# Performance work log

Hardware: AMD Instinct MI355X
Metric: run time of the kernel (lower is better)

Reference implementation:

```python
import jax, jax.numpy as jnp
import numpy as np

N = 100000   # nodes
E = 1600000  # edges (before self-loops)
D_IN = 128
HID = 64
H1 = 4       # heads of conv1
OUT = 2
EPS = 1e-5
NEG_SLOPE = 0.2


def setup_inputs():
    key = jax.random.key(0)
    ks = jax.random.split(key, 12)
    s = 0.1
    return {
        "x": jax.random.normal(ks[0], (N, D_IN), jnp.float32),
        "edge_index": jax.random.randint(ks[1], (2, E), 0, N, jnp.int64),
        "W1": jax.random.normal(ks[2], (D_IN, H1 * HID), jnp.float32) * s,
        "att_src1": jax.random.normal(ks[3], (H1, HID), jnp.float32) * s,
        "att_dst1": jax.random.normal(ks[4], (H1, HID), jnp.float32) * s,
        "b1": jnp.zeros((H1 * HID,), jnp.float32),
        "g1": jnp.ones((H1 * HID,), jnp.float32),
        "be1": jnp.zeros((H1 * HID,), jnp.float32),
        "W2": jax.random.normal(ks[5], (H1 * HID, HID), jnp.float32) * s,
        "att_src2": jax.random.normal(ks[6], (1, HID), jnp.float32) * s,
        "att_dst2": jax.random.normal(ks[7], (1, HID), jnp.float32) * s,
        "b2": jnp.zeros((HID,), jnp.float32),
        "g2": jnp.ones((HID,), jnp.float32),
        "be2": jnp.zeros((HID,), jnp.float32),
        "Wc1": jax.random.normal(ks[8], (HID, HID // 2), jnp.float32) * s,
        "bc1": jnp.zeros((HID // 2,), jnp.float32),
        "Wc2": jax.random.normal(ks[9], (HID // 2, OUT), jnp.float32) * s,
        "bc2": jnp.zeros((OUT,), jnp.float32),
    }


def _gat(x, W, a_src, a_dst, bias, src, dst, heads):
    n = x.shape[0]
    h = (x @ W).reshape(n, heads, -1)              # [N,H,C]
    e_src = jnp.einsum('nhc,hc->nh', h, a_src)     # [N,H]
    e_dst = jnp.einsum('nhc,hc->nh', h, a_dst)
    e = jax.nn.leaky_relu(e_src[src] + e_dst[dst], NEG_SLOPE)  # [Etot,H]
    m = jax.ops.segment_max(e, dst, num_segments=n)            # edge-softmax over incoming
    p = jnp.exp(e - m[dst])
    z = jax.ops.segment_sum(p, dst, num_segments=n)
    alpha = p / z[dst]
    msg = alpha[:, :, None] * h[src]               # [Etot,H,C]
    out = jax.ops.segment_sum(msg, dst, num_segments=n)        # [N,H,C]
    return out.reshape(n, -1) + bias               # concat heads + bias


def _bn(x, g, b):
    m = x.mean(0)
    v = x.var(0)
    return g * (x - m) * jax.lax.rsqrt(v + EPS) + b


def reference(x, edge_index, W1, att_src1, att_dst1, b1, g1, be1,
              W2, att_src2, att_dst2, b2, g2, be2, Wc1, bc1, Wc2, bc2):
    n = x.shape[0]
    loops = jnp.arange(n, dtype=edge_index.dtype)
    src = jnp.concatenate([edge_index[0], loops])  # PyG add_self_loops=True
    dst = jnp.concatenate([edge_index[1], loops])

    h = _gat(x, W1, att_src1, att_dst1, b1, src, dst, H1)
    h = jax.nn.elu(_bn(h, g1, be1))                # dropout = identity (eval)
    h = _gat(h, W2, att_src2, att_dst2, b2, src, dst, 1)
    h = jax.nn.elu(_bn(h, g2, be2))
    h = jax.nn.elu(h @ Wc1 + bc1)
    logits = h @ Wc2 + bc2
    return jax.nn.log_softmax(logits, axis=1)
```

## Files before the change

kernel.cpp:

```cpp
#include <hip/hip_runtime.h>
#include <hip/hip_bf16.h>

constexpr int N_  = 100000;
constexpr int E_  = 1600000;
constexpr int PAD = 48;
constexpr int NBKT = 196;
constexpr int BCAP = 16384;

constexpr size_t P_PARAMS = 8192;
constexpr size_t OFF_WPK1 = 219904;
constexpr size_t OFF_WPK2 = 285440;
constexpr size_t OFF_DEG  = 318464;
constexpr size_t OFF_ES1  = 718464;
constexpr size_t OFF_ED1  = 2318464;
constexpr size_t OFF_ES2  = 3918464;
constexpr size_t OFF_ED2  = 4318464;
constexpr size_t OFF_CSR  = 4718464;
constexpr size_t OFF_H1   = 23918464;
constexpr size_t OFF_H2   = OFF_H1;
constexpr size_t OFF_AGG2 = OFF_H1 + 12800000;
constexpr size_t OFF_AGG1 = 75118464;
constexpr size_t OFF_BCUR = 126318464;
constexpr size_t OFF_BKT  = 126319488;

typedef unsigned short ushortT;
typedef short bf16x8 __attribute__((ext_vector_type(8)));
typedef float f32x4 __attribute__((ext_vector_type(4)));

#define DEV __device__ __forceinline__

DEV float leakyf(float x) { return x > 0.f ? x : 0.2f * x; }
DEV float eluf(float x)   { return x > 0.f ? x : __expf(x) - 1.f; }
DEV float rbf(unsigned short u) { unsigned int b = ((unsigned int)u) << 16; return __uint_as_float(b); }
DEV unsigned short f2b(float f) { __hip_bfloat16 h = __float2bfloat16(f); return *reinterpret_cast<unsigned short*>(&h); }
DEV float sel_head(float4 a, int hd) {
    float r = a.x;
    r = (hd == 1) ? a.y : r;
    r = (hd == 2) ? a.z : r;
    r = (hd == 3) ? a.w : r;
    return r;
}
DEV unsigned short sel_h4(ushort4 u, int hd) {
    unsigned short r = u.x;
    r = (hd == 1) ? u.y : r;
    r = (hd == 2) ? u.z : r;
    r = (hd == 3) ? u.w : r;
    return r;
}
DEV int eread(const int* __restrict__ ei, int mode, int idx) {
    return mode ? ei[(size_t)idx * 2] : ei[idx];
}

__global__ void k_detect2(const int* __restrict__ ei, const unsigned int* __restrict__ g1raw,
                          int* __restrict__ mode, int* __restrict__ fmode) {
    __shared__ int any;
    if (threadIdx.x == 0) any = 0;
    __syncthreads();
    if (ei[2 * threadIdx.x + 1] != 0) atomicOr(&any, 1);
    __syncthreads();
    if (threadIdx.x == 0) {
        *mode = any ? 0 : 1;
        *fmode = (g1raw[0] == 0x3F800000u) ? 0 : 1;
    }
}

struct CvtArgs { const void* src[16]; int off[17]; };
__global__ __launch_bounds__(256) void k_cvtall(CvtArgs a, float* __restrict__ dst,
                                                const int* __restrict__ fmode, int total) {
    int i = blockIdx.x * 256 + threadIdx.x;
    if (i >= total) return;
    int seg = 0;
    #pragma unroll
    for (int s2 = 1; s2 < 16; ++s2) seg += (i >= a.off[s2]);
    int j = i - a.off[seg];
    float v;
    if (*fmode) v = rbf(((const unsigned short*)a.src[seg])[j]);
    else        v = ((const float*)a.src[seg])[j];
    dst[i] = v;
}

__global__ __launch_bounds__(256) void k_packw(const float* __restrict__ pp,
                                               ushortT* __restrict__ w1, ushortT* __restrict__ w2) {
    int i = blockIdx.x * 256 + threadIdx.x;
    if (i < 32768) {
        int j = i & 7, lane = (i >> 3) & 63, ks = (i >> 9) & 3, ct = i >> 11;
        int src = (ks * 32 + ((lane >> 4) << 3) + j) * 256 + ct * 16 + (lane & 15);
        w1[i] = f2b(pp[src]);
    } else if (i < 49152) {
        int i2 = i - 32768;
        int j = i2 & 7, lane = (i2 >> 3) & 63, ks = (i2 >> 9) & 7, ct = i2 >> 12;
        int src = (ks * 32 + ((lane >> 4) << 3) + j) * 64 + ct * 16 + (lane & 15);
        w2[i2] = f2b(pp[34048 + src]);
    }
}

__global__ __launch_bounds__(256) void k_bin(const int* __restrict__ ei, const int* __restrict__ mode,
                                             unsigned int* __restrict__ bucketArr,
                                             int* __restrict__ bucketCursor) {
    __shared__ unsigned int pk[8192];
    __shared__ int cnt[256], scn[256], bse[256], cur[256], gb[256];
    int tid = threadIdx.x;
    cnt[tid] = 0;
    __syncthreads();
    int e0 = blockIdx.x * 8192;
    int m = *mode;
    #pragma unroll 4
    for (int j = 0; j < 32; ++j) {
        int e = e0 + j * 256 + tid;
        if (e < E_) atomicAdd(&cnt[eread(ei, m, E_ + e) >> 9], 1);
    }
    __syncthreads();
    int v = cnt[tid];
    scn[tid] = v;
    __syncthreads();
    for (int d = 1; d < 256; d <<= 1) {
        int t2 = (tid >= d) ? scn[tid - d] : 0;
        __syncthreads();
        scn[tid] += t2;
        __syncthreads();
    }
    int excl = scn[tid] - v;
    bse[tid] = excl;
    cur[tid] = excl;
    __syncthreads();
    #pragma unroll 4
    for (int j = 0; j < 32; ++j) {
        int e = e0 + j * 256 + tid;
        if (e < E_) {
            int s = eread(ei, m, e);
            int d = eread(ei, m, E_ + e);
            int b = d >> 9;
            int p = atomicAdd(&cur[b], 1);
            pk[p] = ((unsigned int)(d & 511) << 17) | (unsigned int)s;
        }
    }
    __syncthreads();
    if (tid < NBKT) {
        int c = cnt[tid];
        gb[tid] = (c > 0) ? atomicAdd(&bucketCursor[tid], c) : 0;
    }
    __syncthreads();
    for (int b = 0; b < NBKT; ++b) {
        int c = cnt[b];
        int lo = bse[b], g = gb[b];
        for (int i = tid; i < c; i += 256) {
            int gi = g + i;
            if (gi < BCAP) bucketArr[(size_t)b * BCAP + gi] = pk[lo + i];
        }
    }
}

__global__ __launch_bounds__(256) void k_csr(const unsigned int* __restrict__ bucketArr,
                                             const int* __restrict__ bucketCursor,
                                             int* __restrict__ csr, int* __restrict__ deg) {
    __shared__ int dl[512];
    int tid = threadIdx.x;
    int b = blockIdx.x;
    int nbase = b * 512;
    int nb = min(N_ - nbase, 512);
    if (nb <= 0) return;
    dl[tid] = 0; dl[tid + 256] = 0;
    __syncthreads();
    int c = min(bucketCursor[b], BCAP);
    const unsigned int* run = bucketArr + (size_t)b * BCAP;
    for (int i = tid; i < c; i += 256) {
        unsigned int p = run[i];
        int s = (int)(p & 0x1FFFFu);
        int dloc = (int)(p >> 17);
        int slot = atomicAdd(&dl[dloc], 1);
        if (slot < PAD - 1) csr[(size_t)(nbase + dloc) * PAD + slot] = s;
    }
    __syncthreads();
    for (int t = tid; t < nb; t += 256) {
        int n = nbase + t;
        int cd = min(dl[t], PAD - 1);
        csr[(size_t)n * PAD + cd] = n;
        deg[n] = cd + 1;
    }
}

__global__ __launch_bounds__(256) void k_gemm1f(const void* __restrict__ x, const int* __restrict__ fmode,
                                                const ushortT* __restrict__ wpk,
                                                const float* __restrict__ as1, const float* __restrict__ ad1,
                                                ushortT* __restrict__ h1,
                                                float* __restrict__ es1, float* __restrict__ ed1) {
    int tid = threadIdx.x, w = tid >> 6, lane = tid & 63;
    int l15 = lane & 15, l4 = lane >> 4;
    int row0 = blockIdx.x * 32;
    int fm = *fmode;
    bf16x8 A[2][4];
    #pragma unroll
    for (int rt = 0; rt < 2; ++rt)
        #pragma unroll
        for (int ks = 0; ks < 4; ++ks) {
            size_t off = (size_t)(row0 + rt * 16 + l15) * 128 + ks * 32 + l4 * 8;
            if (fm) {
                A[rt][ks] = *(const bf16x8*)((const ushortT*)x + off);
            } else {
                const float* xf = (const float*)x + off;
                float4 v0 = *(const float4*)xf;
                float4 v1 = *(const float4*)(xf + 4);
                A[rt][ks] = (bf16x8){(short)f2b(v0.x), (short)f2b(v0.y), (short)f2b(v0.z), (short)f2b(v0.w),
                                     (short)f2b(v1.x), (short)f2b(v1.y), (short)f2b(v1.z), (short)f2b(v1.w)};
            }
        }
    f32x4 acc[2][4];
    #pragma unroll
    for (int rt = 0; rt < 2; ++rt)
        #pragma unroll
        for (int ct = 0; ct < 4; ++ct) acc[rt][ct] = (f32x4){0.f, 0.f, 0.f, 0.f};
    const bf16x8* wp = (const bf16x8*)wpk;
    #pragma unroll
    for (int ct = 0; ct < 4; ++ct) {
        int ctg = w * 4 + ct;
        bf16x8 B0 = wp[(ctg * 4 + 0) * 64 + lane];
        bf16x8 B1 = wp[(ctg * 4 + 1) * 64 + lane];
        bf16x8 B2 = wp[(ctg * 4 + 2) * 64 + lane];
        bf16x8 B3 = wp[(ctg * 4 + 3) * 64 + lane];
        #pragma unroll
        for (int rt = 0; rt < 2; ++rt) {
            acc[rt][ct] = __builtin_amdgcn_mfma_f32_16x16x32_bf16(A[rt][0], B0, acc[rt][ct], 0, 0, 0);
            acc[rt][ct] = __builtin_amdgcn_mfma_f32_16x16x32_bf16(A[rt][1], B1, acc[rt][ct], 0, 0, 0);
            acc[rt][ct] = __builtin_amdgcn_mfma_f32_16x16x32_bf16(A[rt][2], B2, acc[rt][ct], 0, 0, 0);
            acc[rt][ct] = __builtin_amdgcn_mfma_f32_16x16x32_bf16(A[rt][3], B3, acc[rt][ct], 0, 0, 0);
        }
    }
    float asc[4], adc[4];
    #pragma unroll
    for (int ct = 0; ct < 4; ++ct) {
        asc[ct] = as1[w * 64 + ct * 16 + l15];
        adc[ct] = ad1[w * 64 + ct * 16 + l15];
    }
    float pes[2][4], ped[2][4];
    #pragma unroll
    for (int rt = 0; rt < 2; ++rt)
        #pragma unroll
        for (int r = 0; r < 4; ++r) { pes[rt][r] = 0.f; ped[rt][r] = 0.f; }
    #pragma unroll
    for (int rt = 0; rt < 2; ++rt)
        #pragma unroll
        for (int ct = 0; ct < 4; ++ct)
            #pragma unroll
            for (int r = 0; r < 4; ++r) {
                float v = acc[rt][ct][r];
                int row = row0 + rt * 16 + l4 * 4 + r;
                h1[(size_t)row * 256 + w * 64 + ct * 16 + l15] = f2b(v);
                pes[rt][r] = fmaf(v, asc[ct], pes[rt][r]);
                ped[rt][r] = fmaf(v, adc[ct], ped[rt][r]);
            }
    #pragma unroll
    for (int d = 1; d < 16; d <<= 1)
        #pragma unroll
        for (int rt = 0; rt < 2; ++rt)
            #pragma unroll
            for (int r = 0; r < 4; ++r) {
                pes[rt][r] += __shfl_xor(pes[rt][r], d);
                ped[rt][r] += __shfl_xor(ped[rt][r], d);
            }
    if (l15 == 0) {
        #pragma unroll
        for (int rt = 0; rt < 2; ++rt)
            #pragma unroll
            for (int r = 0; r < 4; ++r) {
                int row = row0 + rt * 16 + l4 * 4 + r;
                es1[row * 4 + w] = pes[rt][r];
                ed1[row * 4 + w] = ped[rt][r];
            }
    }
}

__global__ __launch_bounds__(256) void k_lagg1(const ushortT* __restrict__ h1,
                                               const float* __restrict__ es1, const float* __restrict__ ed1,
                                               const int* __restrict__ deg, const int* __restrict__ csr,
                                               const float* __restrict__ b1, ushortT* __restrict__ out) {
    __shared__ int ssrc[4][PAD];
    __shared__ ushort4 sp[4][PAD];
    int wid = threadIdx.x >> 6;
    int lane = threadIdx.x & 63;
    int n = blockIdx.x * 4 + wid;
    int cnt = deg[n];
    int start = n * PAD;
    float4 ed = ((const float4*)ed1)[n];
    float z0 = 0.f, z1 = 0.f, z2 = 0.f, z3 = 0.f;
    if (lane < cnt) {
        int s = csr[start + lane];
        ssrc[wid][lane] = s;
        float4 es = ((const float4*)es1)[s];
        float p0 = __expf(leakyf(es.x + ed.x));
        float p1 = __expf(leakyf(es.y + ed.y));
        float p2 = __expf(leakyf(es.z + ed.z));
        float p3 = __expf(leakyf(es.w + ed.w));
        sp[wid][lane] = make_ushort4(f2b(p0), f2b(p1), f2b(p2), f2b(p3));
        z0 = p0; z1 = p1; z2 = p2; z3 = p3;
    }
    #pragma unroll
    for (int d = 1; d < 64; d <<= 1) {
        z0 += __shfl_xor(z0, d); z1 += __shfl_xor(z1, d);
        z2 += __shfl_xor(z2, d); z3 += __shfl_xor(z3, d);
    }
    int half = lane >> 5, lh = lane & 31, hd = lh >> 3;
    float izh = sel_head(make_float4(1.f / z0, 1.f / z1, 1.f / z2, 1.f / z3), hd);
    float a0 = 0.f, a1 = 0.f, a2 = 0.f, a3 = 0.f, a4 = 0.f, a5 = 0.f, a6 = 0.f, a7 = 0.f;
    float c0 = 0.f, c1 = 0.f, c2 = 0.f, c3 = 0.f, c4 = 0.f, c5 = 0.f, c6 = 0.f, c7 = 0.f;
    int iters = (cnt + 1) >> 1;
    for (int t = 0; t < iters; t += 4) {
        int i0 = 2 * t + half;
        int i1 = i0 + 2, i2 = i0 + 4, i3 = i0 + 6;
        bool v0 = i0 < cnt, v1 = i1 < cnt, v2 = i2 < cnt, v3 = i3 < cnt;
        int s0 = ssrc[wid][v0 ? i0 : 0];
        int s1 = ssrc[wid][v1 ? i1 : 0];
        int s2 = ssrc[wid][v2 ? i2 : 0];
        int s3 = ssrc[wid][v3 ? i3 : 0];
        ushort4 u0 = sp[wid][v0 ? i0 : 0];
        ushort4 u1 = sp[wid][v1 ? i1 : 0];
        ushort4 u2 = sp[wid][v2 ? i2 : 0];
        ushort4 u3 = sp[wid][v3 ? i3 : 0];
        float w0 = v0 ? rbf(sel_h4(u0, hd)) * izh : 0.f;
        float w1 = v1 ? rbf(sel_h4(u1, hd)) * izh : 0.f;
        float w2 = v2 ? rbf(sel_h4(u2, hd)) * izh : 0.f;
        float w3 = v3 ? rbf(sel_h4(u3, hd)) * izh : 0.f;
        uint4 r0 = *(const uint4*)(h1 + (size_t)s0 * 256 + lh * 8);
        uint4 r1 = *(const uint4*)(h1 + (size_t)s1 * 256 + lh * 8);
        uint4 r2 = *(const uint4*)(h1 + (size_t)s2 * 256 + lh * 8);
        uint4 r3 = *(const uint4*)(h1 + (size_t)s3 * 256 + lh * 8);
        a0 = fmaf(w0, rbf((unsigned short)(r0.x & 0xffff)), a0);
        a1 = fmaf(w0, rbf((unsigned short)(r0.x >> 16)), a1);
        a2 = fmaf(w0, rbf((unsigned short)(r0.y & 0xffff)), a2);
        a3 = fmaf(w0, rbf((unsigned short)(r0.y >> 16)), a3);
        a4 = fmaf(w0, rbf((unsigned short)(r0.z & 0xffff)), a4);
        a5 = fmaf(w0, rbf((unsigned short)(r0.z >> 16)), a5);
        a6 = fmaf(w0, rbf((unsigned short)(r0.w & 0xffff)), a6);
        a7 = fmaf(w0, rbf((unsigned short)(r0.w >> 16)), a7);
        c0 = fmaf(w1, rbf((unsigned short)(r1.x & 0xffff)), c0);
        c1 = fmaf(w1, rbf((unsigned short)(r1.x >> 16)), c1);
        c2 = fmaf(w1, rbf((unsigned short)(r1.y & 0xffff)), c2);
        c3 = fmaf(w1, rbf((unsigned short)(r1.y >> 16)), c3);
        c4 = fmaf(w1, rbf((unsigned short)(r1.z & 0xffff)), c4);
        c5 = fmaf(w1, rbf((unsigned short)(r1.z >> 16)), c5);
        c6 = fmaf(w1, rbf((unsigned short)(r1.w & 0xffff)), c6);
        c7 = fmaf(w1, rbf((unsigned short)(r1.w >> 16)), c7);
        a0 = fmaf(w2, rbf((unsigned short)(r2.x & 0xffff)), a0);
        a1 = fmaf(w2, rbf((unsigned short)(r2.x >> 16)), a1);
        a2 = fmaf(w2, rbf((unsigned short)(r2.y & 0xffff)), a2);
        a3 = fmaf(w2, rbf((unsigned short)(r2.y >> 16)), a3);
        a4 = fmaf(w2, rbf((unsigned short)(r2.z & 0xffff)), a4);
        a5 = fmaf(w2, rbf((unsigned short)(r2.z >> 16)), a5);
        a6 = fmaf(w2, rbf((unsigned short)(r2.w & 0xffff)), a6);
        a7 = fmaf(w2, rbf((unsigned short)(r2.w >> 16)), a7);
        c0 = fmaf(w3, rbf((unsigned short)(r3.x & 0xffff)), c0);
        c1 = fmaf(w3, rbf((unsigned short)(r3.x >> 16)), c1);
        c2 = fmaf(w3, rbf((unsigned short)(r3.y & 0xffff)), c2);
        c3 = fmaf(w3, rbf((unsigned short)(r3.y >> 16)), c3);
        c4 = fmaf(w3, rbf((unsigned short)(r3.z & 0xffff)), c4);
        c5 = fmaf(w3, rbf((unsigned short)(r3.z >> 16)), c5);
        c6 = fmaf(w3, rbf((unsigned short)(r3.w & 0xffff)), c6);
        c7 = fmaf(w3, rbf((unsigned short)(r3.w >> 16)), c7);
    }
    a0 += c0; a1 += c1; a2 += c2; a3 += c3; a4 += c4; a5 += c5; a6 += c6; a7 += c7;
    a0 += __shfl_xor(a0, 32); a1 += __shfl_xor(a1, 32);
    a2 += __shfl_xor(a2, 32); a3 += __shfl_xor(a3, 32);
    a4 += __shfl_xor(a4, 32); a5 += __shfl_xor(a5, 32);
    a6 += __shfl_xor(a6, 32); a7 += __shfl_xor(a7, 32);
    if (half == 0) {
        float4 b0 = *(const float4*)(b1 + lh * 8);
        float4 b1v = *(const float4*)(b1 + lh * 8 + 4);
        ushort4 o0 = make_ushort4(f2b(a0 + b0.x), f2b(a1 + b0.y), f2b(a2 + b0.z), f2b(a3 + b0.w));
        ushort4 o1 = make_ushort4(f2b(a4 + b1v.x), f2b(a5 + b1v.y), f2b(a6 + b1v.z), f2b(a7 + b1v.w));
        *(ushort4*)(out + (size_t)n * 256 + lh * 8)     = o0;
        *(ushort4*)(out + (size_t)n * 256 + lh * 8 + 4) = o1;
    }
}

__global__ __launch_bounds__(256) void k_bnstats1(const ushortT* __restrict__ a, double* __restrict__ sums,
                                                  double* __restrict__ sumsq) {
    int c = threadIdx.x;
    int r0 = blockIdx.x * 256;
    int r1 = min(r0 + 256, N_);
    double s = 0.0, q = 0.0;
    for (int r = r0; r < r1; ++r) { float v = rbf(a[(size_t)r * 256 + c]); s += v; q += (double)v * v; }
    atomicAdd(&sums[c], s);
    atomicAdd(&sumsq[c], q);
}

__global__ void k_bnfin(const double* __restrict__ sums, const double* __restrict__ sumsq,
                        const float* __restrict__ g, const float* __restrict__ be,
                        float* __restrict__ s, float* __restrict__ t, int C) {
    int c = threadIdx.x;
    if (c < C) {
        double mean = sums[c] / (double)N_;
        double var = fmax(sumsq[c] / (double)N_ - mean * mean, 0.0);
        double sc = (double)g[c] / sqrt(var + 1e-5);
        s[c] = (float)sc;
        t[c] = (float)((double)be[c] - mean * sc);
    }
}

__global__ __launch_bounds__(256) void k_gemm2f(const ushortT* __restrict__ agg1,
                                                const ushortT* __restrict__ wpk2,
                                                const float* __restrict__ sc1, const float* __restrict__ tc1,
                                                const float* __restrict__ as2, const float* __restrict__ ad2,
                                                ushortT* __restrict__ h2,
                                                float* __restrict__ es2, float* __restrict__ ed2) {
    int tid = threadIdx.x, w = tid >> 6, lane = tid & 63;
    int l15 = lane & 15, l4 = lane >> 4;
    int row0 = blockIdx.x * 64;
    int arow = row0 + w * 16 + l15;
    int ar = min(arow, N_ - 1);
    bf16x8 A[8];
    #pragma unroll
    for (int ks = 0; ks < 8; ++ks) {
        const ushortT* ap = agg1 + (size_t)ar * 256 + ks * 32 + l4 * 8;
        int pi = ks * 32 + l4 * 8;
        uint4 u = *(const uint4*)ap;
        float4 s0 = *(const float4*)(sc1 + pi);
        float4 s1 = *(const float4*)(sc1 + pi + 4);
        float4 t0 = *(const float4*)(tc1 + pi);
        float4 t1 = *(const float4*)(tc1 + pi + 4);
        float e0 = eluf(fmaf(rbf((unsigned short)(u.x & 0xffff)), s0.x, t0.x));
        float e1 = eluf(fmaf(rbf((unsigned short)(u.x >> 16)),    s0.y, t0.y));
        float e2 = eluf(fmaf(rbf((unsigned short)(u.y & 0xffff)), s0.z, t0.z));
        float e3 = eluf(fmaf(rbf((unsigned short)(u.y >> 16)),    s0.w, t0.w));
        float e4 = eluf(fmaf(rbf((unsigned short)(u.z & 0xffff)), s1.x, t1.x));
        float e5 = eluf(fmaf(rbf((unsigned short)(u.z >> 16)),    s1.y, t1.y));
        float e6 = eluf(fmaf(rbf((unsigned short)(u.w & 0xffff)), s1.z, t1.z));
        float e7 = eluf(fmaf(rbf((unsigned short)(u.w >> 16)),    s1.w, t1.w));
        A[ks] = (bf16x8){(short)f2b(e0), (short)f2b(e1), (short)f2b(e2), (short)f2b(e3),
                         (short)f2b(e4), (short)f2b(e5), (short)f2b(e6), (short)f2b(e7)};
    }
    f32x4 acc[4];
    #pragma unroll
    for (int ct = 0; ct < 4; ++ct) acc[ct] = (f32x4){0.f, 0.f, 0.f, 0.f};
    const bf16x8* wp = (const bf16x8*)wpk2;
    #pragma unroll
    for (int ct = 0; ct < 4; ++ct) {
        #pragma unroll
        for (int ks = 0; ks < 8; ++ks) {
            bf16x8 B = wp[(ct * 8 + ks) * 64 + lane];
            acc[ct] = __builtin_amdgcn_mfma_f32_16x16x32_bf16(A[ks], B, acc[ct], 0, 0, 0);
        }
    }
    float asc[4], adc[4];
    #pragma unroll
    for (int ct = 0; ct < 4; ++ct) {
        asc[ct] = as2[ct * 16 + l15];
        adc[ct] = ad2[ct * 16 + l15];
    }
    float pes[4] = {0.f, 0.f, 0.f, 0.f}, ped[4] = {0.f, 0.f, 0.f, 0.f};
    #pragma unroll
    for (int ct = 0; ct < 4; ++ct)
        #pragma unroll
        for (int r = 0; r < 4; ++r) {
            float v = acc[ct][r];
            int row = row0 + w * 16 + l4 * 4 + r;
            if (row < N_) h2[(size_t)row * 64 + ct * 16 + l15] = f2b(v);
            pes[r] = fmaf(v, asc[ct], pes[r]);
            ped[r] = fmaf(v, adc[ct], ped[r]);
        }
    #pragma unroll
    for (int d = 1; d < 16; d <<= 1)
        #pragma unroll
        for (int r = 0; r < 4; ++r) {
            pes[r] += __shfl_xor(pes[r], d);
            ped[r] += __shfl_xor(ped[r], d);
        }
    if (l15 == 0) {
        #pragma unroll
        for (int r = 0; r < 4; ++r) {
            int row = row0 + w * 16 + l4 * 4 + r;
            if (row < N_) { es2[row] = pes[r]; ed2[row] = ped[r]; }
        }
    }
}

__global__ __launch_bounds__(256) void k_lagg2(const ushortT* __restrict__ h2,
                                               const float* __restrict__ es2, const float* __restrict__ ed2,
                                               const int* __restrict__ deg, const int* __restrict__ csr,
                                               const float* __restrict__ b2, float* __restrict__ out) {
    __shared__ int ssrc[4][PAD];
    __shared__ float sp[4][PAD];
    int wid = threadIdx.x >> 6;
    int lane = threadIdx.x & 63;
    int n = blockIdx.x * 4 + wid;
    int cnt = deg[n];
    int start = n * PAD;
    float ed = ed2[n];
    float z = 0.f;
    if (lane < cnt) {
        int s = csr[start + lane];
        ssrc[wid][lane] = s;
        float p = __expf(leakyf(es2[s] + ed));
        sp[wid][lane] = p;
        z = p;
    }
    #pragma unroll
    for (int d = 1; d < 64; d <<= 1) z += __shfl_xor(z, d);
    float iz = 1.f / z;
    int half = lane >> 5, lh = lane & 31;
    float a0 = 0.f, a1 = 0.f, c0 = 0.f, c1 = 0.f;
    int iters = (cnt + 1) >> 1;
    for (int t = 0; t < iters; t += 4) {
        int i0 = 2 * t + half;
        int i1 = i0 + 2, i2 = i0 + 4, i3 = i0 + 6;
        bool v0 = i0 < cnt, v1 = i1 < cnt, v2 = i2 < cnt, v3 = i3 < cnt;
        int s0 = ssrc[wid][v0 ? i0 : 0];
        int s1 = ssrc[wid][v1 ? i1 : 0];
        int s2 = ssrc[wid][v2 ? i2 : 0];
        int s3 = ssrc[wid][v3 ? i3 : 0];
        float w0 = v0 ? sp[wid][i0] * iz : 0.f;
        float w1 = v1 ? sp[wid][i1] * iz : 0.f;
        float w2 = v2 ? sp[wid][i2] * iz : 0.f;
        float w3 = v3 ? sp[wid][i3] * iz : 0.f;
        unsigned int u0 = *(const unsigned int*)(h2 + (size_t)s0 * 64 + lh * 2);
        unsigned int u1 = *(const unsigned int*)(h2 + (size_t)s1 * 64 + lh * 2);
        unsigned int u2 = *(const unsigned int*)(h2 + (size_t)s2 * 64 + lh * 2);
        unsigned int u3 = *(const unsigned int*)(h2 + (size_t)s3 * 64 + lh * 2);
        a0 = fmaf(w0, rbf((unsigned short)(u0 & 0xffff)), a0);
        a1 = fmaf(w0, rbf((unsigned short)(u0 >> 16)), a1);
        c0 = fmaf(w1, rbf((unsigned short)(u1 & 0xffff)), c0);
        c1 = fmaf(w1, rbf((unsigned short)(u1 >> 16)), c1);
        a0 = fmaf(w2, rbf((unsigned short)(u2 & 0xffff)), a0);
        a1 = fmaf(w2, rbf((unsigned short)(u2 >> 16)), a1);
        c0 = fmaf(w3, rbf((unsigned short)(u3 & 0xffff)), c0);
        c1 = fmaf(w3, rbf((unsigned short)(u3 >> 16)), c1);
    }
    a0 += c0; a1 += c1;
    a0 += __shfl_xor(a0, 32);
    a1 += __shfl_xor(a1, 32);
    if (half == 0) {
        out[(size_t)n * 64 + lh * 2 + 0] = a0 + b2[lh * 2 + 0];
        out[(size_t)n * 64 + lh * 2 + 1] = a1 + b2[lh * 2 + 1];
    }
}

__global__ __launch_bounds__(256) void k_bnstats2(const float* __restrict__ a, double* __restrict__ sums,
                                                  double* __restrict__ sumsq) {
    __shared__ double sm[256], sq[256];
    int tid = threadIdx.x;
    int c = tid & 63, rr = tid >> 6;
    int r0 = blockIdx.x * 1024;
    int r1 = min(r0 + 1024, N_);
    double s = 0.0, q = 0.0;
    for (int r = r0 + rr; r < r1; r += 4) { float v = a[(size_t)r * 64 + c]; s += v; q += (double)v * v; }
    sm[tid] = s; sq[tid] = q; __syncthreads();
    if (tid < 64) {
        s = sm[tid] + sm[tid + 64] + sm[tid + 128] + sm[tid + 192];
        q = sq[tid] + sq[tid + 64] + sq[tid + 128] + sq[tid + 192];
        atomicAdd(&sums[tid], s);
        atomicAdd(&sumsq[tid], q);
    }
}

__global__ __launch_bounds__(256) void k_cls(const float* __restrict__ agg2, const float* __restrict__ Wc1,
                                             const float* __restrict__ bc1, const float* __restrict__ Wc2,
                                             const float* __restrict__ bc2, const float* __restrict__ s2,
                                             const float* __restrict__ t2, float* __restrict__ out) {
    __shared__ float w1s[2048];
    __shared__ float w2s[64];
    __shared__ float b1s[32];
    __shared__ float b2s[2];
    __shared__ float ss[64], ts[64];
    int tid = threadIdx.x;
    for (int i = tid; i < 2048; i += 256) w1s[i] = Wc1[i];
    if (tid < 64) { w2s[tid] = Wc2[tid]; ss[tid] = s2[tid]; ts[tid] = t2[tid]; }
    if (tid < 32) b1s[tid] = bc1[tid];
    if (tid < 2)  b2s[tid] = bc2[tid];
    __syncthreads();
    int n = blockIdx.x * 256 + tid;
    if (n >= N_) return;
    float hv[64];
    const float4* rp = (const float4*)(agg2 + (size_t)n * 64);
    #pragma unroll
    for (int q = 0; q < 16; ++q) {
        float4 v = rp[q];
        float tmp[4] = {v.x, v.y, v.z, v.w};
        #pragma unroll
        for (int c4 = 0; c4 < 4; ++c4) {
            int c = q * 4 + c4;
            hv[c] = eluf(fmaf(tmp[c4], ss[c], ts[c]));
        }
    }
    float l0 = b2s[0], l1 = b2s[1];
    for (int j = 0; j < 32; ++j) {
        float a = b1s[j];
        #pragma unroll
        for (int k = 0; k < 64; ++k) a = fmaf(hv[k], w1s[k * 32 + j], a);
        float u = eluf(a);
        l0 = fmaf(u, w2s[j * 2 + 0], l0);
        l1 = fmaf(u, w2s[j * 2 + 1], l1);
    }
    float mx = fmaxf(l0, l1);
    float lse = mx + __logf(__expf(l0 - mx) + __expf(l1 - mx));
    out[(size_t)n * 2 + 0] = l0 - lse;
    out[(size_t)n * 2 + 1] = l1 - lse;
}

extern "C" void kernel_launch(void* const* d_in, const int* in_sizes, int n_in,
                              void* d_out, int out_size, void* d_ws, size_t ws_size,
                              hipStream_t stream) {
    float* out = (float*)d_out;

    char* ws = (char*)d_ws;
    double* sums1  = (double*)(ws + 0);
    double* sumsq1 = (double*)(ws + 2048);
    double* sums2  = (double*)(ws + 4096);
    double* sumsq2 = (double*)(ws + 4608);
    float* s1 = (float*)(ws + 5120), *t1 = (float*)(ws + 6144);
    float* s2 = (float*)(ws + 7168), *t2 = (float*)(ws + 7424);
    int* mode  = (int*)(ws + 7936);
    int* fmode = (int*)(ws + 7940);

    float* pp   = (float*)(ws + P_PARAMS);
    float* as1f = pp + 32768;
    float* ad1f = pp + 33024;
    float* b1f  = pp + 33280;
    float* g1f  = pp + 33536;
    float* be1f = pp + 33792;
    float* as2f = pp + 50432;
    float* ad2f = pp + 50496;
    float* b2f  = pp + 50560;
    float* g2f  = pp + 50624;
    float* be2f = pp + 50688;
    float* Wc1f = pp + 50752;
    float* bc1f = pp + 52800;
    float* Wc2f = pp + 52832;
    float* bc2f = pp + 52896;
    const int CV_TOTAL = 52898;

    ushortT* wpk1 = (ushortT*)(ws + OFF_WPK1);
    ushortT* wpk2 = (ushortT*)(ws + OFF_WPK2);
    int* deg    = (int*)(ws + OFF_DEG);
    int* csr    = (int*)(ws + OFF_CSR);
    float* es1  = (float*)(ws + OFF_ES1);
    float* ed1  = (float*)(ws + OFF_ED1);
    float* es2  = (float*)(ws + OFF_ES2);
    float* ed2  = (float*)(ws + OFF_ED2);
    ushortT* h1 = (ushortT*)(ws + OFF_H1);
    ushortT* h2 = (ushortT*)(ws + OFF_H2);
    float* agg2 = (float*)(ws + OFF_AGG2);
    ushortT* agg1 = (ushortT*)(ws + OFF_AGG1);
    int* bcur = (int*)(ws + OFF_BCUR);
    unsigned int* bkt = (unsigned int*)(ws + OFF_BKT);

    hipMemsetAsync(ws, 0, 5120, stream);
    hipMemsetAsync(bcur, 0, 1024, stream);
    k_detect2<<<1, 256, 0, stream>>>((const int*)d_in[1], (const unsigned int*)d_in[6], mode, fmode);

    CvtArgs ca;
    const int srcIdx[16] = {2,3,4,5,6,7,8,9,10,11,12,13,14,15,16,17};
    const int offsEl[17] = {0,32768,33024,33280,33536,33792,34048,50432,50496,50560,
                            50624,50688,50752,52800,52832,52896,52898};
    for (int i = 0; i < 16; ++i) ca.src[i] = d_in[srcIdx[i]];
    for (int i = 0; i < 17; ++i) ca.off[i] = offsEl[i];
    k_cvtall<<<(CV_TOTAL + 255) / 256, 256, 0, stream>>>(ca, pp, fmode, CV_TOTAL);
    k_packw <<<192, 256, 0, stream>>>(pp, wpk1, wpk2);

    k_bin<<<(E_ + 8191) / 8192, 256, 0, stream>>>((const int*)d_in[1], mode, bkt, bcur);
    k_csr<<<NBKT, 256, 0, stream>>>(bkt, bcur, csr, deg);

    k_gemm1f<<<N_ / 32, 256, 0, stream>>>(d_in[0], fmode, wpk1, as1f, ad1f, h1, es1, ed1);
    k_lagg1<<<N_ / 4, 256, 0, stream>>>(h1, es1, ed1, deg, csr, b1f, agg1);
    k_bnstats1<<<(N_ + 255) / 256, 256, 0, stream>>>(agg1, sums1, sumsq1);
    k_bnfin<<<1, 256, 0, stream>>>(sums1, sumsq1, g1f, be1f, s1, t1, 256);

    k_gemm2f<<<(N_ + 63) / 64, 256, 0, stream>>>(agg1, wpk2, s1, t1, as2f, ad2f, h2, es2, ed2);
    k_lagg2<<<N_ / 4, 256, 0, stream>>>(h2, es2, ed2, deg, csr, b2f, agg2);
    k_bnstats2<<<98, 256, 0, stream>>>(agg2, sums2, sumsq2);
    k_bnfin<<<1, 64, 0, stream>>>(sums2, sumsq2, g2f, be2f, s2, t2, 64);

    k_cls<<<(N_ + 255) / 256, 256, 0, stream>>>(agg2, Wc1f, bc1f, Wc2f, bc2f, s2, t2, out);
}
```

Baseline: 517.3 us.

## Stage GEMM1 input tile in LDS, per-wave bucket flush, merge memsets

GEMM1 now loads its 32x128 input tile into shared memory with coalesced row-contiguous loads (and bf16 conversion) before building the MFMA operands, instead of each lane gathering strided rows directly from global memory. The binning kernel's flush loop assigns buckets to waves rather than looping all 256 threads over every bucket, which cuts idle lanes and per-bucket barrier-free overhead. The bucket cursor moves into the low workspace region so that one memset replaces two. These changes add an LDS round-trip and a barrier in GEMM1.

```diff
diff --git a/kernel.cpp b/kernel.cpp
--- a/kernel.cpp
+++ b/kernel.cpp
@@ -7,21 +7,20 @@
 constexpr int NBKT = 196;
 constexpr int BCAP = 16384;
 
-constexpr size_t P_PARAMS = 8192;
-constexpr size_t OFF_WPK1 = 219904;
-constexpr size_t OFF_WPK2 = 285440;
-constexpr size_t OFF_DEG  = 318464;
-constexpr size_t OFF_ES1  = 718464;
-constexpr size_t OFF_ED1  = 2318464;
-constexpr size_t OFF_ES2  = 3918464;
-constexpr size_t OFF_ED2  = 4318464;
-constexpr size_t OFF_CSR  = 4718464;
-constexpr size_t OFF_H1   = 23918464;
+constexpr size_t P_PARAMS = 12288;
+constexpr size_t OFF_WPK1 = 224000;
+constexpr size_t OFF_WPK2 = 289536;
+constexpr size_t OFF_DEG  = 322304;
+constexpr size_t OFF_ES1  = 722304;
+constexpr size_t OFF_ED1  = 2322304;
+constexpr size_t OFF_ES2  = 3922304;
+constexpr size_t OFF_ED2  = 4322304;
+constexpr size_t OFF_CSR  = 4722304;
+constexpr size_t OFF_H1   = 23922304;
 constexpr size_t OFF_H2   = OFF_H1;
 constexpr size_t OFF_AGG2 = OFF_H1 + 12800000;
-constexpr size_t OFF_AGG1 = 75118464;
-constexpr size_t OFF_BCUR = 126318464;
-constexpr size_t OFF_BKT  = 126319488;
+constexpr size_t OFF_AGG1 = 75122304;
+constexpr size_t OFF_BKT  = 126322304;
 
 typedef unsigned short ushortT;
 typedef short bf16x8 __attribute__((ext_vector_type(8)));
@@ -140,10 +139,11 @@
         gb[tid] = (c > 0) ? atomicAdd(&bucketCursor[tid], c) : 0;
     }
     __syncthreads();
-    for (int b = 0; b < NBKT; ++b) {
+    int wv = tid >> 6, ln = tid & 63;
+    for (int b = wv; b < NBKT; b += 4) {
         int c = cnt[b];
         int lo = bse[b], g = gb[b];
-        for (int i = tid; i < c; i += 256) {
+        for (int i = ln; i < c; i += 64) {
             int gi = g + i;
             if (gi < BCAP) bucketArr[(size_t)b * BCAP + gi] = pk[lo + i];
         }
@@ -184,26 +184,36 @@
                                                 const float* __restrict__ as1, const float* __restrict__ ad1,
                                                 ushortT* __restrict__ h1,
                                                 float* __restrict__ es1, float* __restrict__ ed1) {
+    __shared__ ushortT xs[32][132];
     int tid = threadIdx.x, w = tid >> 6, lane = tid & 63;
     int l15 = lane & 15, l4 = lane >> 4;
     int row0 = blockIdx.x * 32;
-    int fm = *fmode;
+    if (*fmode) {
+        const ushortT* xg = (const ushortT*)x + (size_t)row0 * 128;
+        for (int i = tid; i < 512; i += 256) {
+            int r = i >> 4, cc = (i & 15) * 8;
+            ushort4 a = *(const ushort4*)(xg + r * 128 + cc);
+            ushort4 b = *(const ushort4*)(xg + r * 128 + cc + 4);
+            *(ushort4*)&xs[r][cc]     = a;
+            *(ushort4*)&xs[r][cc + 4] = b;
+        }
+    } else {
+        const float* xg = (const float*)x + (size_t)row0 * 128;
+        for (int i = tid; i < 512; i += 256) {
+            int r = i >> 4, cc = (i & 15) * 8;
+            float4 a = *(const float4*)(xg + r * 128 + cc);
+            float4 b = *(const float4*)(xg + r * 128 + cc + 4);
+            *(ushort4*)&xs[r][cc]     = make_ushort4(f2b(a.x), f2b(a.y), f2b(a.z), f2b(a.w));
+            *(ushort4*)&xs[r][cc + 4] = make_ushort4(f2b(b.x), f2b(b.y), f2b(b.z), f2b(b.w));
+        }
+    }
+    __syncthreads();
     bf16x8 A[2][4];
     #pragma unroll
     for (int rt = 0; rt < 2; ++rt)
         #pragma unroll
-        for (int ks = 0; ks < 4; ++ks) {
-            size_t off = (size_t)(row0 + rt * 16 + l15) * 128 + ks * 32 + l4 * 8;
-            if (fm) {
-                A[rt][ks] = *(const bf16x8*)((const ushortT*)x + off);
-            } else {
-                const float* xf = (const float*)x + off;
-                float4 v0 = *(const float4*)xf;
-                float4 v1 = *(const float4*)(xf + 4);
-                A[rt][ks] = (bf16x8){(short)f2b(v0.x), (short)f2b(v0.y), (short)f2b(v0.z), (short)f2b(v0.w),
-                                     (short)f2b(v1.x), (short)f2b(v1.y), (short)f2b(v1.z), (short)f2b(v1.w)};
-            }
-        }
+        for (int ks = 0; ks < 4; ++ks)
+            A[rt][ks] = *(const bf16x8*)&xs[rt * 16 + l15][ks * 32 + l4 * 8];
     f32x4 acc[2][4];
     #pragma unroll
     for (int rt = 0; rt < 2; ++rt)
@@ -604,10 +614,11 @@
     double* sumsq1 = (double*)(ws + 2048);
     double* sums2  = (double*)(ws + 4096);
     double* sumsq2 = (double*)(ws + 4608);
-    float* s1 = (float*)(ws + 5120), *t1 = (float*)(ws + 6144);
-    float* s2 = (float*)(ws + 7168), *t2 = (float*)(ws + 7424);
-    int* mode  = (int*)(ws + 7936);
-    int* fmode = (int*)(ws + 7940);
+    int* bcur = (int*)(ws + 5120);
+    float* s1 = (float*)(ws + 6144), *t1 = (float*)(ws + 7168);
+    float* s2 = (float*)(ws + 8192), *t2 = (float*)(ws + 8448);
+    int* mode  = (int*)(ws + 8704);
+    int* fmode = (int*)(ws + 8708);
 
     float* pp   = (float*)(ws + P_PARAMS);
     float* as1f = pp + 32768;
@@ -638,11 +649,9 @@
     ushortT* h2 = (ushortT*)(ws + OFF_H2);
     float* agg2 = (float*)(ws + OFF_AGG2);
     ushortT* agg1 = (ushortT*)(ws + OFF_AGG1);
-    int* bcur = (int*)(ws + OFF_BCUR);
     unsigned int* bkt = (unsigned int*)(ws + OFF_BKT);
 
-    hipMemsetAsync(ws, 0, 5120, stream);
-    hipMemsetAsync(bcur, 0, 1024, stream);
+    hipMemsetAsync(ws, 0, 6144, stream);
     k_detect2<<<1, 256, 0, stream>>>((const int*)d_in[1], (const unsigned int*)d_in[6], mode, fmode);
 
     CvtArgs ca;
```

Result: faster. 473.3 us (-8.5%).
